# Performance work log

Measured on AMD Instinct MI355X. Metric: run time of the kernel, lower is better.

## Reference

```python
import jax, jax.numpy as jnp
from jax import lax
import numpy as np

D = 128          # condition_dim
NUM_STEPS = 1000
FFN = 2048       # torch TransformerEncoderLayer default dim_feedforward


def _conv(x, w, b):
    # 3x3 conv, stride 1, padding 1 (SAME), NCHW / OIHW layout as in torch
    y = lax.conv_general_dilated(x, w, (1, 1), 'SAME',
                                 dimension_numbers=('NCHW', 'OIHW', 'NCHW'))
    return y + b[None, :, None, None]


def _ln(x, g, b):
    m = jnp.mean(x, -1, keepdims=True)
    v = jnp.mean((x - m) ** 2, -1, keepdims=True)
    return (x - m) / jnp.sqrt(v + 1e-5) * g + b


def setup_inputs() -> dict:
    key = jax.random.key(0)
    ks = iter(jax.random.split(key, 40))
    B, C, H, W = 64, 3, 128, 128
    flat = C * H * W
    def rn(shape, scale=0.02):
        return jax.random.normal(next(ks), shape, jnp.float32) * scale
    return dict(
        cond_img=jax.random.normal(next(ks), (B, C, H, W), jnp.float32),
        tgt_img=jax.random.normal(next(ks), (B, C, H, W), jnp.float32),
        noise=jax.random.normal(next(ks), (B, C, H, W), jnp.float32),
        t=jax.random.randint(next(ks), (B,), 0, NUM_STEPS),
        # condition encoder params
        enc_lin_w=rn((D, flat)), enc_lin_b=jnp.zeros((D,), jnp.float32),
        in_w=rn((2, 3 * D, D)), in_b=jnp.zeros((2, 3 * D), jnp.float32),
        out_w=rn((2, D, D)), out_b=jnp.zeros((2, D), jnp.float32),
        ff1_w=rn((2, FFN, D)), ff1_b=jnp.zeros((2, FFN), jnp.float32),
        ff2_w=rn((2, D, FFN)), ff2_b=jnp.zeros((2, D), jnp.float32),
        ln1_g=jnp.ones((2, D), jnp.float32), ln1_b=jnp.zeros((2, D), jnp.float32),
        ln2_g=jnp.ones((2, D), jnp.float32), ln2_b=jnp.zeros((2, D), jnp.float32),
        # SimpleUNet params
        d1_w=rn((32, C, 3, 3)), d1_b=jnp.zeros((32,), jnp.float32),
        d2_w=rn((64, 32, 3, 3)), d2_b=jnp.zeros((64,), jnp.float32),
        mid_w=rn((64, D)), mid_b=jnp.zeros((64,), jnp.float32),
        u1_w=rn((32, 64, 3, 3)), u1_b=jnp.zeros((32,), jnp.float32),
        u2_w=rn((C, 32, 3, 3)), u2_b=jnp.zeros((C,), jnp.float32),
    )


def _forward(cond_img, tgt_img, noise, t,
             enc_lin_w, enc_lin_b, in_w, in_b, out_w, out_b,
             ff1_w, ff1_b, ff2_w, ff2_b, ln1_g, ln1_b, ln2_g, ln2_b,
             d1_w, d1_b, d2_w, d2_b, mid_w, mid_b, u1_w, u1_b, u2_w, u2_b):
    B = cond_img.shape[0]
    # ---- TransformerConditionEncoder (seq_len == 1, eval mode) ----
    x = cond_img.reshape(B, -1) @ enc_lin_w.T + enc_lin_b  # [B, D]
    for i in range(2):
        # self-attention over a length-1 sequence: softmax over one key == 1,
        # so attn(x) == out_proj(v_proj(x)) exactly.
        v = x @ in_w[i][2 * D:3 * D].T + in_b[i][2 * D:3 * D]
        a = v @ out_w[i].T + out_b[i]
        x = _ln(x + a, ln1_g[i], ln1_b[i])
        f = jnp.maximum(x @ ff1_w[i].T + ff1_b[i], 0.0) @ ff2_w[i].T + ff2_b[i]
        x = _ln(x + f, ln2_g[i], ln2_b[i])
    c = x  # [B, D]
    # ---- LinearScheduler.q_sample ----
    betas = jnp.linspace(1e-4, 0.02, NUM_STEPS)
    alpha_bars = jnp.cumprod(1.0 - betas)
    ab = alpha_bars[t][:, None, None, None]
    z_t = jnp.sqrt(ab) * tgt_img + jnp.sqrt(1.0 - ab) * noise
    # ---- SimpleUNet ----
    h = jax.nn.relu(_conv(z_t, d1_w, d1_b))
    h = jax.nn.relu(_conv(h, d2_w, d2_b))
    h = h + (c @ mid_w.T + mid_b)[:, :, None, None]
    h = jax.nn.relu(_conv(h, u1_w, u1_b))
    eps_pred = _conv(h, u2_w, u2_b)
    # ---- MSE loss ----
    return jnp.mean((eps_pred - noise) ** 2)


def reference(cond_img, tgt_img, noise, t,
              enc_lin_w, enc_lin_b, in_w, in_b, out_w, out_b,
              ff1_w, ff1_b, ff2_w, ff2_b, ln1_g, ln1_b, ln2_g, ln2_b,
              d1_w, d1_b, d2_w, d2_b, mid_w, mid_b, u1_w, u1_b, u2_w, u2_b):
    return _forward(cond_img, tgt_img, noise, t,
                    enc_lin_w, enc_lin_b, in_w, in_b, out_w, out_b,
                    ff1_w, ff1_b, ff2_w, ff2_b, ln1_g, ln1_b, ln2_g, ln2_b,
                    d1_w, d1_b, d2_w, d2_b, mid_w, mid_b, u1_w, u1_b, u2_w, u2_b)
```

## Files before the change

### kernel.cpp

```cpp
#include <hip/hip_runtime.h>
#include <math.h>

#define ENC_K 49152
#define KSEG 64
#define KLEN (ENC_K / KSEG)

typedef __attribute__((ext_vector_type(8))) short bf16x8;
typedef __attribute__((ext_vector_type(4))) float f32x4;

__device__ inline unsigned short f2bf(float f) {
    unsigned int u = __builtin_bit_cast(unsigned int, f);
    unsigned int r = u + 0x7fffu + ((u >> 16) & 1u);
    return (unsigned short)(r >> 16);
}
__device__ inline float bf2f(unsigned short h) {
    return __builtin_bit_cast(float, ((unsigned int)h) << 16);
}
__device__ inline float dot4(const float4 a, const float4 b) {
    return a.x * b.x + a.y * b.y + a.z * b.z + a.w * b.w;
}

__device__ inline int xcd_work(int total) {
    int orig = blockIdx.x + gridDim.x * (blockIdx.y + gridDim.y * blockIdx.z);
    return (orig & 7) * (total >> 3) + (orig >> 3);
}

__global__ void k_alpha(const int* __restrict__ t, float* __restrict__ sab, float* __restrict__ snab) {
    int b = threadIdx.x;
    if (b < 64) {
        int tb = t[b];
        const float step = (0.02f - 1e-4f) / 999.0f;
        float ab = 1.0f;
        for (int i = 0; i <= tb; ++i) {
            float beta = 1e-4f + step * (float)i;
            ab *= (1.0f - beta);
        }
        sab[b] = sqrtf(ab);
        snab[b] = sqrtf(1.0f - ab);
    }
}

__global__ void k_prep_cw(const float* __restrict__ w, unsigned short* __restrict__ out, int CO, int CI) {
    int idx = blockIdx.x * 256 + threadIdx.x;
    int total = CO * CI * 9;
    if (idx < total) {
        int tap = idx / (CO * CI);
        int rem = idx % (CO * CI);
        int co = rem / CI, ci = rem % CI;
        out[idx] = f2bf(w[((size_t)co * CI + ci) * 9 + tap]);
    }
}

__global__ void k_prep_u2(const float* __restrict__ w, unsigned short* __restrict__ out) {
    int idx = blockIdx.x * 256 + threadIdx.x;
    if (idx < 9 * 16 * 32) {
        int tap = idx / 512;
        int rem = idx % 512;
        int co = rem / 32, ci = rem % 32;
        out[idx] = (co < 3) ? f2bf(w[((size_t)co * 32 + ci) * 9 + tap]) : (unsigned short)0;
    }
}

__global__ void k_prep_bf(const float* __restrict__ in, unsigned short* __restrict__ out, int n) {
    int i = blockIdx.x * 256 + threadIdx.x;
    if (i < n) out[i] = f2bf(in[i]);
}

__global__ void k_enc_gemm(const float* __restrict__ cond, const float* __restrict__ w,
                           float* __restrict__ partial) {
    __shared__ float As[32][68];
    __shared__ float Ws[32][68];
    int tid = threadIdx.x;
    int j = tid & 15, i = tid >> 4;
    int d0 = blockIdx.x * 32, b0 = blockIdx.y * 32;
    int k0 = blockIdx.z * KLEN;
    float a00 = 0.f, a01 = 0.f, a10 = 0.f, a11 = 0.f;
    for (int kk = 0; kk < KLEN; kk += 64) {
        for (int idx = tid; idx < 512; idx += 256) {
            int r = idx >> 4, c = (idx & 15) << 2;
            *(float4*)&As[r][c] = *(const float4*)&cond[(size_t)(b0 + r) * ENC_K + k0 + kk + c];
            *(float4*)&Ws[r][c] = *(const float4*)&w[(size_t)(d0 + r) * ENC_K + k0 + kk + c];
        }
        __syncthreads();
        const float4* aA = (const float4*)&As[i][0];
        const float4* aB = (const float4*)&As[i + 16][0];
        const float4* wA = (const float4*)&Ws[j][0];
        const float4* wB = (const float4*)&Ws[j + 16][0];
#pragma unroll
        for (int k = 0; k < 16; ++k) {
            float4 av0 = aA[k], av1 = aB[k], wv0 = wA[k], wv1 = wB[k];
            a00 += dot4(av0, wv0); a01 += dot4(av0, wv1);
            a10 += dot4(av1, wv0); a11 += dot4(av1, wv1);
        }
        __syncthreads();
    }
    size_t base = (size_t)blockIdx.z * 64;
    partial[(base + b0 + i) * 128 + d0 + j] = a00;
    partial[(base + b0 + i) * 128 + d0 + j + 16] = a01;
    partial[(base + b0 + i + 16) * 128 + d0 + j] = a10;
    partial[(base + b0 + i + 16) * 128 + d0 + j + 16] = a11;
}

__global__ void k_enc_reduce(const float* __restrict__ partial, const float* __restrict__ bias,
                             float* __restrict__ x0) {
    int idx = blockIdx.x * 256 + threadIdx.x;
    float s = bias[idx & 127];
    for (int ks = 0; ks < KSEG; ++ks) s += partial[(size_t)ks * 8192 + idx];
    x0[idx] = s;
}

__device__ float sum128(float v, int tid, float* red) {
    if (tid < 128) red[tid] = v;
    __syncthreads();
    if (tid < 64) red[tid] += red[tid + 64]; __syncthreads();
    if (tid < 32) red[tid] += red[tid + 32]; __syncthreads();
    if (tid < 16) red[tid] += red[tid + 16]; __syncthreads();
    if (tid < 8)  red[tid] += red[tid + 8];  __syncthreads();
    if (tid < 4)  red[tid] += red[tid + 4];  __syncthreads();
    if (tid < 2)  red[tid] += red[tid + 2];  __syncthreads();
    if (tid < 1)  red[tid] += red[tid + 1];  __syncthreads();
    float s = red[0];
    __syncthreads();
    return s;
}

__global__ __launch_bounds__(512) void k_tf_attn(
    const float* __restrict__ xs, float* __restrict__ yo,
    const float* __restrict__ in_w, const float* __restrict__ in_b,
    const float* __restrict__ out_w, const float* __restrict__ out_b,
    const float* __restrict__ ln1_g, const float* __restrict__ ln1_b, int L) {
    __shared__ float xr[128], vr[128], tp[4][128], red[128];
    int b = blockIdx.x, tid = threadIdx.x;
    if (tid < 128) xr[tid] = xs[b * 128 + tid];
    __syncthreads();
    int d = tid & 127, s = tid >> 7;
    {
        const float4* w = (const float4*)(in_w + ((size_t)L * 384 + 256 + d) * 128) + s * 8;
        const float4* x4 = (const float4*)xr + s * 8;
        float p = 0.f;
#pragma unroll
        for (int k = 0; k < 8; ++k) p += dot4(x4[k], w[k]);
        tp[s][d] = p;
    }
    __syncthreads();
    if (tid < 128) vr[tid] = in_b[L * 384 + 256 + tid] + tp[0][tid] + tp[1][tid] + tp[2][tid] + tp[3][tid];
    __syncthreads();
    {
        const float4* w = (const float4*)(out_w + ((size_t)L * 128 + d) * 128) + s * 8;
        const float4* v4 = (const float4*)vr + s * 8;
        float p = 0.f;
#pragma unroll
        for (int k = 0; k < 8; ++k) p += dot4(v4[k], w[k]);
        tp[s][d] = p;
    }
    __syncthreads();
    float y = 0.f;
    if (tid < 128) y = xr[tid] + out_b[L * 128 + tid] + tp[0][tid] + tp[1][tid] + tp[2][tid] + tp[3][tid];
    float m1 = sum128(y, tid, red) * (1.f / 128.f);
    float c1 = y - m1;
    float v1 = sum128(c1 * c1, tid, red) * (1.f / 128.f);
    if (tid < 128)
        yo[b * 128 + tid] = c1 * rsqrtf(v1 + 1e-5f) * ln1_g[L * 128 + tid] + ln1_b[L * 128 + tid];
}

__global__ __launch_bounds__(256, 2) void k_ff1m(
    const float* __restrict__ yo, const unsigned short* __restrict__ w1b,
    const float* __restrict__ ff1_b, unsigned short* __restrict__ f1, int L) {
    __shared__ __align__(16) unsigned short xs[64 * 136];
    int tid = threadIdx.x;
    int lane = tid & 63, wv = tid >> 6, l15 = lane & 15, ch = lane >> 4;
    int n0 = blockIdx.x * 64 + wv * 16;
    for (int e = tid; e < 8192; e += 256)
        xs[(e >> 7) * 136 + (e & 127)] = f2bf(yo[e]);
    __syncthreads();
    f32x4 acc[4];
    f32x4 zf = {0.f, 0.f, 0.f, 0.f};
#pragma unroll
    for (int rg = 0; rg < 4; ++rg) acc[rg] = zf;
    const unsigned short* wrow = w1b + ((size_t)L * 2048 + n0 + l15) * 128 + ch * 8;
#pragma unroll
    for (int ks = 0; ks < 4; ++ks) {
        bf16x8 af = *(const bf16x8*)(wrow + ks * 32);
#pragma unroll
        for (int rg = 0; rg < 4; ++rg) {
            bf16x8 bv = *(const bf16x8*)(xs + (rg * 16 + l15) * 136 + ks * 32 + ch * 8);
            acc[rg] = __builtin_amdgcn_mfma_f32_16x16x32_bf16(af, bv, acc[rg], 0, 0, 0);
        }
    }
#pragma unroll
    for (int rg = 0; rg < 4; ++rg) {
        ushort4 o;
#pragma unroll
        for (int r = 0; r < 4; ++r)
            ((unsigned short*)&o)[r] =
                f2bf(fmaxf(acc[rg][r] + ff1_b[L * 2048 + n0 + ch * 4 + r], 0.f));
        *(ushort4*)(f1 + (size_t)(rg * 16 + l15) * 2056 + n0 + ch * 4) = o;
    }
}

__global__ __launch_bounds__(256, 2) void k_ff2m(
    const unsigned short* __restrict__ f1, const unsigned short* __restrict__ w2b,
    float* __restrict__ part, int L) {
    int tid = threadIdx.x;
    int lane = tid & 63, wv = tid >> 6, l15 = lane & 15, ch = lane >> 4;
    int ks = blockIdx.x;
    int dw = blockIdx.y * 64 + wv * 16;
    f32x4 acc[4];
    f32x4 zf = {0.f, 0.f, 0.f, 0.f};
#pragma unroll
    for (int rg = 0; rg < 4; ++rg) acc[rg] = zf;
    const unsigned short* wrow = w2b + ((size_t)L * 128 + dw + l15) * 2048 + ks * 512 + ch * 8;
    const unsigned short* frow = f1 + ks * 512 + ch * 8;
#pragma unroll
    for (int kst = 0; kst < 16; ++kst) {
        bf16x8 af = *(const bf16x8*)(wrow + kst * 32);
#pragma unroll
        for (int rg = 0; rg < 4; ++rg) {
            bf16x8 bv = *(const bf16x8*)(frow + (size_t)(rg * 16 + l15) * 2056 + kst * 32);
            acc[rg] = __builtin_amdgcn_mfma_f32_16x16x32_bf16(af, bv, acc[rg], 0, 0, 0);
        }
    }
#pragma unroll
    for (int rg = 0; rg < 4; ++rg)
        *(float4*)&part[((size_t)ks * 64 + rg * 16 + l15) * 128 + dw + ch * 4] = *(float4*)&acc[rg];
}

__global__ __launch_bounds__(128) void k_tf_red(
    const float* __restrict__ part, const float* __restrict__ yo,
    float* __restrict__ xs, const float* __restrict__ ff2_b,
    const float* __restrict__ ln2_g, const float* __restrict__ ln2_b, int L) {
    __shared__ float red[128];
    int b = blockIdx.x, tid = threadIdx.x;
    float y2 = yo[b * 128 + tid] + ff2_b[L * 128 + tid];
#pragma unroll
    for (int ks = 0; ks < 4; ++ks) y2 += part[((size_t)ks * 64 + b) * 128 + tid];
    float m2 = sum128(y2, tid, red) * (1.f / 128.f);
    float c2 = y2 - m2;
    float v2 = sum128(c2 * c2, tid, red) * (1.f / 128.f);
    xs[b * 128 + tid] = c2 * rsqrtf(v2 + 1e-5f) * ln2_g[L * 128 + tid] + ln2_b[L * 128 + tid];
}

__global__ void k_mid(const float* __restrict__ xe, const float* __restrict__ mid_w,
                      const float* __restrict__ mid_b, float* __restrict__ mid) {
    int b = blockIdx.x, c = threadIdx.x;
    float s = mid_b[c];
    const float* xr = xe + b * 128;
    const float* wr = mid_w + c * 128;
    for (int k = 0; k < 128; ++k) s += xr[k] * wr[k];
    mid[b * 64 + c] = s;
}

__global__ __launch_bounds__(256, 4) void k_conv1(
    const float* __restrict__ tgt, const float* __restrict__ noise,
    const float* __restrict__ sab, const float* __restrict__ snab,
    const float* __restrict__ wgt, const float* __restrict__ bias,
    unsigned short* __restrict__ h1, int b0) {
    __shared__ float it[3][18][35];
    __shared__ float wt[16][3][9];
    int tid = threadIdx.x;
    int tx = tid & 15, ty = tid >> 4;
    int total = gridDim.x * gridDim.y * gridDim.z;
    int w = xcd_work(total);
    int bx = w % gridDim.x; int t2 = w / gridDim.x;
    int by = t2 % gridDim.y; int bz = t2 / gridDim.y;
    int bl = bz >> 1, g = bz & 1;
    int bg = b0 + bl, co0 = g * 16;
    float za = sab[bg], zb = snab[bg];
    for (int idx = tid; idx < 3 * 18 * 34; idx += 256) {
        int c = idx / (18 * 34), rem = idx % (18 * 34);
        int yy = rem / 34, xx = rem % 34;
        int gy = by * 16 + yy - 1, gx = bx * 32 + xx - 1;
        float v = 0.f;
        if (gy >= 0 && gy < 128 && gx >= 0 && gx < 128) {
            size_t off = (((size_t)bg * 3 + c) * 128 + gy) * 128 + gx;
            v = za * tgt[off] + zb * noise[off];
        }
        it[c][yy][xx] = v;
    }
    for (int idx = tid; idx < 16 * 27; idx += 256) {
        int co = idx / 27, rem = idx % 27;
        wt[co][rem / 9][rem % 9] = wgt[(size_t)(co0 + co) * 27 + rem];
    }
    __syncthreads();
    float acc[16][2];
#pragma unroll
    for (int co = 0; co < 16; ++co) { acc[co][0] = 0.f; acc[co][1] = 0.f; }
#pragma unroll
    for (int c = 0; c < 3; ++c)
#pragma unroll
        for (int ky = 0; ky < 3; ++ky) {
            float win[4];
#pragma unroll
            for (int i = 0; i < 4; ++i) win[i] = it[c][ty + ky][tx * 2 + i];
#pragma unroll
            for (int kx = 0; kx < 3; ++kx)
#pragma unroll
                for (int co = 0; co < 16; ++co) {
                    float ww = wt[co][c][ky * 3 + kx];
                    acc[co][0] += win[kx] * ww;
                    acc[co][1] += win[kx + 1] * ww;
                }
        }
    int gy = by * 16 + ty, gx0 = bx * 32 + tx * 2;
#pragma unroll
    for (int p = 0; p < 2; ++p) {
        __attribute__((aligned(16))) unsigned short ov[16];
#pragma unroll
        for (int co = 0; co < 16; ++co)
            ov[co] = f2bf(fmaxf(acc[co][p] + bias[co0 + co], 0.f));
        size_t o = (((size_t)bl * 128 + gy) * 128 + gx0 + p) * 32 + co0;
        *(float4*)(h1 + o) = *(float4*)&ov[0];
        *(float4*)(h1 + o + 8) = *(float4*)&ov[8];
    }
}

template <int CIN, int COB, int COUT, int MOUT>
__global__ __launch_bounds__(256, 2) void k_convMg(
    const unsigned short* __restrict__ in, const unsigned short* __restrict__ wb,
    const float* __restrict__ bias, const float* __restrict__ mid,
    unsigned short* __restrict__ out, int b0) {
    const int GROUPS = COUT / (16 * COB);
    __shared__ __align__(16) unsigned short in_t[10 * 34 * 40];
    __shared__ __align__(16) unsigned short w_t[9 * COB * 16 * 40];
    int tid = threadIdx.x;
    int total = gridDim.x * gridDim.y * gridDim.z;
    int wk = xcd_work(total);
    int bx = wk % gridDim.x; int t2 = wk / gridDim.x;
    int by = t2 % gridDim.y; int bz = t2 / gridDim.y;
    int bl = bz / GROUPS, g = bz % GROUPS;
    int bg = b0 + bl;
    int co0 = g * COB * 16;
    int lane = tid & 63, wv = tid >> 6;
    int l15 = lane & 15, ch = lane >> 4;

    f32x4 acc[2][2][COB];
    f32x4 zf = {0.f, 0.f, 0.f, 0.f};
#pragma unroll
    for (int a = 0; a < 2; ++a)
#pragma unroll
        for (int bq = 0; bq < 2; ++bq)
#pragma unroll
            for (int c = 0; c < COB; ++c) acc[a][bq][c] = zf;

    for (int cs = 0; cs < CIN / 32; ++cs) {
        if (cs) __syncthreads();
        for (int c = tid; c < 10 * 34 * 4; c += 256) {
            int cc = c & 3, pix = c >> 2;
            int xx = pix % 34, yy = pix / 34;
            int gy = by * 8 + yy - 1, gx = bx * 32 + xx - 1;
            bf16x8 v = {0, 0, 0, 0, 0, 0, 0, 0};
            if (gy >= 0 && gy < 128 && gx >= 0 && gx < 128)
                v = *(const bf16x8*)(in + (((size_t)bl * 128 + gy) * 128 + gx) * CIN + cs * 32 + cc * 8);
            *(bf16x8*)(in_t + pix * 40 + cc * 8) = v;
        }
        for (int c = tid; c < 9 * COB * 16 * 4; c += 256) {
            int cc = c & 3, row = c >> 2;
            int tap = row / (COB * 16), co = row % (COB * 16);
            bf16x8 v = *(const bf16x8*)(wb + ((size_t)(tap * COUT + co0 + co)) * CIN + cs * 32 + cc * 8);
            *(bf16x8*)(w_t + row * 40 + cc * 8) = v;
        }
        __syncthreads();
#pragma unroll
        for (int ky = 0; ky < 3; ++ky)
#pragma unroll
            for (int kx = 0; kx < 3; ++kx) {
                int tap = ky * 3 + kx;
                bf16x8 af[COB];
#pragma unroll
                for (int cb = 0; cb < COB; ++cb)
                    af[cb] = *(const bf16x8*)(w_t + (tap * COB * 16 + cb * 16 + l15) * 40 + ch * 8);
#pragma unroll
                for (int yl = 0; yl < 2; ++yl) {
                    int yloc = 2 * wv + yl + ky;
#pragma unroll
                    for (int xt = 0; xt < 2; ++xt) {
                        int xloc = xt * 16 + l15 + kx;
                        bf16x8 bfv = *(const bf16x8*)(in_t + (yloc * 34 + xloc) * 40 + ch * 8);
#pragma unroll
                        for (int cb = 0; cb < COB; ++cb)
                            acc[yl][xt][cb] = __builtin_amdgcn_mfma_f32_16x16x32_bf16(
                                af[cb], bfv, acc[yl][xt][cb], 0, 0, 0);
                    }
                }
            }
    }
#pragma unroll
    for (int yl = 0; yl < 2; ++yl) {
        int gy = by * 8 + 2 * wv + yl;
#pragma unroll
        for (int xt = 0; xt < 2; ++xt) {
            int gx = bx * 32 + xt * 16 + l15;
            size_t pixo = (((size_t)bl * 128 + gy) * 128 + gx) * COUT;
#pragma unroll
            for (int cb = 0; cb < COB; ++cb) {
                int co = co0 + cb * 16 + ch * 4;
                ushort4 o;
#pragma unroll
                for (int r = 0; r < 4; ++r) {
                    float v = acc[yl][xt][cb][r] + bias[co + r];
                    v = fmaxf(v, 0.f);
                    if (MOUT == 2) v += mid[bg * 64 + co + r];
                    ((unsigned short*)&o)[r] = f2bf(v);
                }
                *(ushort4*)(out + pixo + co) = o;
            }
        }
    }
}

__global__ __launch_bounds__(256, 3) void k_u2m(
    const unsigned short* __restrict__ h3, const unsigned short* __restrict__ wbu2,
    const float* __restrict__ u2_b, const float* __restrict__ noise,
    float* __restrict__ partial, int b0) {
    __shared__ __align__(16) unsigned short in_t[340 * 40];
    __shared__ __align__(16) unsigned short w_t[9 * 16 * 40];
    __shared__ float rs[256];
    int tid = threadIdx.x;
    int total = gridDim.x * gridDim.y * gridDim.z;
    int wk = xcd_work(total);
    int bx = wk % gridDim.x; int t2 = wk / gridDim.x;
    int by = t2 % gridDim.y; int bl = t2 / gridDim.y;
    int bg = b0 + bl;
    int lane = tid & 63, wv = tid >> 6, l15 = lane & 15, ch = lane >> 4;

    for (int c = tid; c < 340 * 4; c += 256) {
        int cc = c & 3, pix = c >> 2;
        int xx = pix % 34, yy = pix / 34;
        int gy = by * 8 + yy - 1, gx = bx * 32 + xx - 1;
        bf16x8 v = {0, 0, 0, 0, 0, 0, 0, 0};
        if (gy >= 0 && gy < 128 && gx >= 0 && gx < 128)
            v = *(const bf16x8*)(h3 + (((size_t)bl * 128 + gy) * 128 + gx) * 32 + cc * 8);
        *(bf16x8*)(in_t + pix * 40 + cc * 8) = v;
    }
    for (int c = tid; c < 9 * 16 * 4; c += 256) {
        int cc = c & 3, row = c >> 2;
        bf16x8 v = *(const bf16x8*)(wbu2 + (size_t)row * 32 + cc * 8);
        *(bf16x8*)(w_t + row * 40 + cc * 8) = v;
    }
    __syncthreads();

    f32x4 acc[2][2];
    f32x4 zf = {0.f, 0.f, 0.f, 0.f};
    acc[0][0] = zf; acc[0][1] = zf; acc[1][0] = zf; acc[1][1] = zf;
#pragma unroll
    for (int ky = 0; ky < 3; ++ky)
#pragma unroll
        for (int kx = 0; kx < 3; ++kx) {
            int tap = ky * 3 + kx;
            bf16x8 af = *(const bf16x8*)(w_t + (tap * 16 + l15) * 40 + ch * 8);
#pragma unroll
            for (int yl = 0; yl < 2; ++yl) {
                int yloc = 2 * wv + yl + ky;
#pragma unroll
                for (int xt = 0; xt < 2; ++xt) {
                    int xloc = xt * 16 + l15 + kx;
                    bf16x8 bfv = *(const bf16x8*)(in_t + (yloc * 34 + xloc) * 40 + ch * 8);
                    acc[yl][xt] = __builtin_amdgcn_mfma_f32_16x16x32_bf16(af, bfv, acc[yl][xt], 0, 0, 0);
                }
            }
        }
    float ss = 0.f;
    if (ch == 0) {
#pragma unroll
        for (int yl = 0; yl < 2; ++yl) {
            int gy = by * 8 + 2 * wv + yl;
#pragma unroll
            for (int xt = 0; xt < 2; ++xt) {
                int gx = bx * 32 + xt * 16 + l15;
#pragma unroll
                for (int r = 0; r < 3; ++r) {
                    float v = acc[yl][xt][r] + u2_b[r];
                    float d = v - noise[(((size_t)bg * 3 + r) * 128 + gy) * 128 + gx];
                    ss += d * d;
                }
            }
        }
    }
    rs[tid] = ss;
    __syncthreads();
    for (int s = 128; s > 0; s >>= 1) {
        if (tid < s) rs[tid] += rs[tid + s];
        __syncthreads();
    }
    if (tid == 0) partial[bg * 64 + by * 4 + bx] = rs[0];
}

__global__ void k_final(const float* __restrict__ partial, float* __restrict__ out) {
    __shared__ float rs[256];
    int tid = threadIdx.x;
    float s = 0.f;
    for (int i = tid; i < 4096; i += 256) s += partial[i];
    rs[tid] = s;
    __syncthreads();
    for (int st = 128; st > 0; st >>= 1) {
        if (tid < st) rs[tid] += rs[tid + st];
        __syncthreads();
    }
    if (tid == 0) out[0] = rs[0] / 3145728.0f;
}

extern "C" void kernel_launch(void* const* d_in, const int* in_sizes, int n_in,
                              void* d_out, int out_size, void* d_ws, size_t ws_size,
                              hipStream_t stream) {
    const float* cond   = (const float*)d_in[0];
    const float* tgt    = (const float*)d_in[1];
    const float* noise  = (const float*)d_in[2];
    const int*   t      = (const int*)d_in[3];
    const float* enc_w  = (const float*)d_in[4];
    const float* enc_b  = (const float*)d_in[5];
    const float* in_w   = (const float*)d_in[6];
    const float* in_b   = (const float*)d_in[7];
    const float* out_w  = (const float*)d_in[8];
    const float* out_b  = (const float*)d_in[9];
    const float* ff1_w  = (const float*)d_in[10];
    const float* ff1_b  = (const float*)d_in[11];
    const float* ff2_w  = (const float*)d_in[12];
    const float* ff2_b  = (const float*)d_in[13];
    const float* ln1_g  = (const float*)d_in[14];
    const float* ln1_b  = (const float*)d_in[15];
    const float* ln2_g  = (const float*)d_in[16];
    const float* ln2_b  = (const float*)d_in[17];
    const float* d1_w   = (const float*)d_in[18];
    const float* d1_b   = (const float*)d_in[19];
    const float* d2_w   = (const float*)d_in[20];
    const float* d2_b   = (const float*)d_in[21];
    const float* mid_w  = (const float*)d_in[22];
    const float* mid_b  = (const float*)d_in[23];
    const float* u1_w   = (const float*)d_in[24];
    const float* u1_b   = (const float*)d_in[25];
    const float* u2_w   = (const float*)d_in[26];
    const float* u2_b   = (const float*)d_in[27];

    float* ws = (float*)d_ws;
    float* sab     = ws;
    float* snab    = ws + 64;
    float* x0      = ws + 128;
    float* mid     = ws + 16512;
    float* msepart = ws + 86144;
    unsigned short* wb2  = (unsigned short*)(ws + 90240);
    unsigned short* wbu1 = (unsigned short*)(ws + 99456);
    unsigned short* wbu2 = (unsigned short*)(ws + 108672);

    const size_t SMALL = 131072;
    const size_t ENCP = (size_t)KSEG * 8192;
    float* encpart = ws + SMALL;
    float* tfy     = encpart + ENCP;
    unsigned short* tff1 = (unsigned short*)(tfy + 8192);
    float* tfpart  = tfy + 8192 + 65792;
    unsigned short* wbf1 = (unsigned short*)(tfpart + 32768);
    unsigned short* wbf2 = (unsigned short*)(tfpart + 32768 + 262144);

    size_t fixed = SMALL + ENCP + 8192 + 65792 + 32768 + 262144 + 262144;
    size_t avail = (ws_size / 4 > fixed) ? (ws_size / 4 - fixed) : 0;
    int NB = 1;
    const int cands[7] = {64, 32, 16, 8, 4, 2, 1};
    for (int ci = 0; ci < 7; ++ci) {
        if ((size_t)cands[ci] * 1048576ull <= avail) { NB = cands[ci]; break; }
    }
    unsigned short* hb1 = (unsigned short*)(ws + fixed);
    unsigned short* hb2 = (unsigned short*)(ws + fixed + (size_t)NB * 262144ull);
    unsigned short* hb3 = (unsigned short*)(ws + fixed + (size_t)NB * 786432ull);

    k_alpha<<<1, 64, 0, stream>>>(t, sab, snab);
    k_prep_cw<<<72, 256, 0, stream>>>(d2_w, wb2, 64, 32);
    k_prep_cw<<<72, 256, 0, stream>>>(u1_w, wbu1, 32, 64);
    k_prep_u2<<<18, 256, 0, stream>>>(u2_w, wbu2);
    k_prep_bf<<<2048, 256, 0, stream>>>(ff1_w, wbf1, 524288);
    k_prep_bf<<<2048, 256, 0, stream>>>(ff2_w, wbf2, 524288);
    k_enc_gemm<<<dim3(4, 2, KSEG), 256, 0, stream>>>(cond, enc_w, encpart);
    k_enc_reduce<<<32, 256, 0, stream>>>(encpart, enc_b, x0);
    for (int L = 0; L < 2; ++L) {
        k_tf_attn<<<64, 512, 0, stream>>>(x0, tfy, in_w, in_b, out_w, out_b, ln1_g, ln1_b, L);
        k_ff1m<<<32, 256, 0, stream>>>(tfy, wbf1, ff1_b, tff1, L);
        k_ff2m<<<dim3(4, 2), 256, 0, stream>>>(tff1, wbf2, tfpart, L);
        k_tf_red<<<64, 128, 0, stream>>>(tfpart, tfy, x0, ff2_b, ln2_g, ln2_b, L);
    }
    k_mid<<<64, 64, 0, stream>>>(x0, mid_w, mid_b, mid);

    for (int cb = 0; cb < 64; cb += NB) {
        k_conv1<<<dim3(4, 8, NB * 2), 256, 0, stream>>>(
            tgt, noise, sab, snab, d1_w, d1_b, hb1, cb);
        k_convMg<32, 4, 64, 2><<<dim3(4, 16, NB), 256, 0, stream>>>(
            hb1, wb2, d2_b, mid, hb2, cb);
        k_convMg<64, 2, 32, 1><<<dim3(4, 16, NB), 256, 0, stream>>>(
            hb2, wbu1, u1_b, nullptr, hb3, cb);
        k_u2m<<<dim3(4, 16, NB), 256, 0, stream>>>(
            hb3, wbu2, u2_b, noise, msepart, cb);
    }

    k_final<<<1, 256, 0, stream>>>(msepart, (float*)d_out);
}
```

Baseline: 388.1 us.

## Store h2/h3 activations in FP8 and run u1/u2 convs with FP8 MFMA

The d2 conv now writes its output as packed FP8 instead of bf16. A new FP8 conv kernel for u1 reads that output and writes h3 in FP8, and the u2+MSE kernel now uses FP8 MFMA with FP8 weights. This halves activation traffic for the two intermediate buffers, halves LDS footprint, and uses the higher-throughput FP8 matrix instructions. The trade-off is much lower activation and weight precision, which may push the MSE loss outside tolerance.

```diff
diff --git a/kernel.cpp b/kernel.cpp
--- a/kernel.cpp
+++ b/kernel.cpp
@@ -13,11 +13,17 @@
     unsigned int r = u + 0x7fffu + ((u >> 16) & 1u);
     return (unsigned short)(r >> 16);
 }
-__device__ inline float bf2f(unsigned short h) {
-    return __builtin_bit_cast(float, ((unsigned int)h) << 16);
-}
 __device__ inline float dot4(const float4 a, const float4 b) {
     return a.x * b.x + a.y * b.y + a.z * b.z + a.w * b.w;
+}
+__device__ inline unsigned int pk4_fp8(float a, float b, float c, float d) {
+    int v = 0;
+    v = __builtin_amdgcn_cvt_pk_fp8_f32(a, b, v, false);
+    v = __builtin_amdgcn_cvt_pk_fp8_f32(c, d, v, true);
+    return (unsigned int)v;
+}
+__device__ inline f32x4 mfma_fp8(unsigned long long a, unsigned long long b, f32x4 c) {
+    return __builtin_amdgcn_mfma_f32_16x16x32_fp8_fp8((long)a, (long)b, c, 0, 0, 0);
 }
 
 __device__ inline int xcd_work(int total) {
@@ -51,13 +57,25 @@
     }
 }
 
-__global__ void k_prep_u2(const float* __restrict__ w, unsigned short* __restrict__ out) {
+__global__ void k_prep_u1f8(const float* __restrict__ w, unsigned char* __restrict__ out) {
     int idx = blockIdx.x * 256 + threadIdx.x;
-    if (idx < 9 * 16 * 32) {
-        int tap = idx / 512;
-        int rem = idx % 512;
-        int co = rem / 32, ci = rem % 32;
-        out[idx] = (co < 3) ? f2bf(w[((size_t)co * 32 + ci) * 9 + tap]) : (unsigned short)0;
+    if (idx < 18432) {
+        int tap = idx / 2048, rem = idx % 2048;
+        int co = rem >> 6, ci = rem & 63;
+        float f = w[((size_t)co * 64 + ci) * 9 + tap];
+        int v = __builtin_amdgcn_cvt_pk_fp8_f32(f, 0.f, 0, false);
+        out[idx] = (unsigned char)(v & 0xFF);
+    }
+}
+
+__global__ void k_prep_u2f8(const float* __restrict__ w, unsigned char* __restrict__ out) {
+    int idx = blockIdx.x * 256 + threadIdx.x;
+    if (idx < 4608) {
+        int tap = idx / 512, rem = idx % 512;
+        int co = rem >> 5, ci = rem & 31;
+        float f = (co < 3) ? w[((size_t)co * 32 + ci) * 9 + tap] : 0.f;
+        int v = __builtin_amdgcn_cvt_pk_fp8_f32(f, 0.f, 0, false);
+        out[idx] = (unsigned char)(v & 0xFF);
     }
 }
 
@@ -314,7 +332,7 @@
     }
 }
 
-template <int CIN, int COB, int COUT, int MOUT>
+template <int CIN, int COB, int COUT, int MOUT, int OF8>
 __global__ __launch_bounds__(256, 2) void k_convMg(
     const unsigned short* __restrict__ in, const unsigned short* __restrict__ wb,
     const float* __restrict__ bias, const float* __restrict__ mid,
@@ -394,26 +412,117 @@
 #pragma unroll
             for (int cb = 0; cb < COB; ++cb) {
                 int co = co0 + cb * 16 + ch * 4;
-                ushort4 o;
+                float vv[4];
 #pragma unroll
                 for (int r = 0; r < 4; ++r) {
                     float v = acc[yl][xt][cb][r] + bias[co + r];
                     v = fmaxf(v, 0.f);
                     if (MOUT == 2) v += mid[bg * 64 + co + r];
-                    ((unsigned short*)&o)[r] = f2bf(v);
+                    vv[r] = v;
                 }
-                *(ushort4*)(out + pixo + co) = o;
+                if (OF8) {
+                    unsigned int pk = pk4_fp8(vv[0], vv[1], vv[2], vv[3]);
+                    *(unsigned int*)((unsigned char*)out + pixo + co) = pk;
+                } else {
+                    ushort4 o;
+#pragma unroll
+                    for (int r = 0; r < 4; ++r) ((unsigned short*)&o)[r] = f2bf(vv[r]);
+                    *(ushort4*)(out + pixo + co) = o;
+                }
             }
         }
     }
 }
 
-__global__ __launch_bounds__(256, 3) void k_u2m(
-    const unsigned short* __restrict__ h3, const unsigned short* __restrict__ wbu2,
+__global__ __launch_bounds__(256, 3) void k_convF8u1(
+    const unsigned char* __restrict__ h2, const unsigned char* __restrict__ wb,
+    const float* __restrict__ bias, unsigned char* __restrict__ h3, int b0) {
+    __shared__ __align__(16) unsigned char in_t[340 * 72];
+    __shared__ __align__(16) unsigned char w_t[288 * 72];
+    int tid = threadIdx.x;
+    int total = gridDim.x * gridDim.y * gridDim.z;
+    int wk = xcd_work(total);
+    int bx = wk % gridDim.x; int t2 = wk / gridDim.x;
+    int by = t2 % gridDim.y; int bl = t2 / gridDim.y;
+    int lane = tid & 63, wv = tid >> 6, l15 = lane & 15, ch = lane >> 4;
+
+    for (int c = tid; c < 340 * 8; c += 256) {
+        int cc = c & 7, pix = c >> 3;
+        int xx = pix % 34, yy = pix / 34;
+        int gy = by * 8 + yy - 1, gx = bx * 32 + xx - 1;
+        unsigned long long v = 0ull;
+        if (gy >= 0 && gy < 128 && gx >= 0 && gx < 128)
+            v = *(const unsigned long long*)(h2 + (((size_t)bl * 128 + gy) * 128 + gx) * 64 + cc * 8);
+        *(unsigned long long*)(in_t + pix * 72 + cc * 8) = v;
+    }
+    for (int c = tid; c < 288 * 8; c += 256) {
+        int cc = c & 7, row = c >> 3;
+        *(unsigned long long*)(w_t + row * 72 + cc * 8) =
+            *(const unsigned long long*)(wb + (size_t)row * 64 + cc * 8);
+    }
+    __syncthreads();
+
+    f32x4 acc[2][2][2];
+    f32x4 zf = {0.f, 0.f, 0.f, 0.f};
+#pragma unroll
+    for (int a = 0; a < 2; ++a)
+#pragma unroll
+        for (int bq = 0; bq < 2; ++bq)
+#pragma unroll
+            for (int c = 0; c < 2; ++c) acc[a][bq][c] = zf;
+
+#pragma unroll
+    for (int cs = 0; cs < 2; ++cs)
+#pragma unroll
+        for (int ky = 0; ky < 3; ++ky)
+#pragma unroll
+            for (int kx = 0; kx < 3; ++kx) {
+                int tap = ky * 3 + kx;
+                unsigned long long A[2];
+#pragma unroll
+                for (int cb = 0; cb < 2; ++cb)
+                    A[cb] = *(const unsigned long long*)(
+                        w_t + (tap * 32 + cb * 16 + l15) * 72 + cs * 32 + ch * 8);
+#pragma unroll
+                for (int yl = 0; yl < 2; ++yl) {
+                    int yloc = 2 * wv + yl + ky;
+#pragma unroll
+                    for (int xt = 0; xt < 2; ++xt) {
+                        int xloc = xt * 16 + l15 + kx;
+                        unsigned long long B = *(const unsigned long long*)(
+                            in_t + (yloc * 34 + xloc) * 72 + cs * 32 + ch * 8);
+#pragma unroll
+                        for (int cb = 0; cb < 2; ++cb)
+                            acc[yl][xt][cb] = mfma_fp8(A[cb], B, acc[yl][xt][cb]);
+                    }
+                }
+            }
+#pragma unroll
+    for (int yl = 0; yl < 2; ++yl) {
+        int gy = by * 8 + 2 * wv + yl;
+#pragma unroll
+        for (int xt = 0; xt < 2; ++xt) {
+            int gx = bx * 32 + xt * 16 + l15;
+            size_t pixo = (((size_t)bl * 128 + gy) * 128 + gx) * 32;
+#pragma unroll
+            for (int cb = 0; cb < 2; ++cb) {
+                int co = cb * 16 + ch * 4;
+                float v0 = fmaxf(acc[yl][xt][cb][0] + bias[co], 0.f);
+                float v1 = fmaxf(acc[yl][xt][cb][1] + bias[co + 1], 0.f);
+                float v2 = fmaxf(acc[yl][xt][cb][2] + bias[co + 2], 0.f);
+                float v3 = fmaxf(acc[yl][xt][cb][3] + bias[co + 3], 0.f);
+                *(unsigned int*)(h3 + pixo + co) = pk4_fp8(v0, v1, v2, v3);
+            }
+        }
+    }
+}
+
+__global__ __launch_bounds__(256, 3) void k_u2f8(
+    const unsigned char* __restrict__ h3, const unsigned char* __restrict__ wbu2,
     const float* __restrict__ u2_b, const float* __restrict__ noise,
     float* __restrict__ partial, int b0) {
-    __shared__ __align__(16) unsigned short in_t[340 * 40];
-    __shared__ __align__(16) unsigned short w_t[9 * 16 * 40];
+    __shared__ __align__(16) unsigned char in_t[340 * 40];
+    __shared__ __align__(16) unsigned char w_t[144 * 40];
     __shared__ float rs[256];
     int tid = threadIdx.x;
     int total = gridDim.x * gridDim.y * gridDim.z;
@@ -427,15 +536,15 @@
         int cc = c & 3, pix = c >> 2;
         int xx = pix % 34, yy = pix / 34;
         int gy = by * 8 + yy - 1, gx = bx * 32 + xx - 1;
-        bf16x8 v = {0, 0, 0, 0, 0, 0, 0, 0};
+        unsigned long long v = 0ull;
         if (gy >= 0 && gy < 128 && gx >= 0 && gx < 128)
-            v = *(const bf16x8*)(h3 + (((size_t)bl * 128 + gy) * 128 + gx) * 32 + cc * 8);
-        *(bf16x8*)(in_t + pix * 40 + cc * 8) = v;
-    }
-    for (int c = tid; c < 9 * 16 * 4; c += 256) {
+            v = *(const unsigned long long*)(h3 + (((size_t)bl * 128 + gy) * 128 + gx) * 32 + cc * 8);
+        *(unsigned long long*)(in_t + pix * 40 + cc * 8) = v;
+    }
+    for (int c = tid; c < 144 * 4; c += 256) {
         int cc = c & 3, row = c >> 2;
-        bf16x8 v = *(const bf16x8*)(wbu2 + (size_t)row * 32 + cc * 8);
-        *(bf16x8*)(w_t + row * 40 + cc * 8) = v;
+        *(unsigned long long*)(w_t + row * 40 + cc * 8) =
+            *(const unsigned long long*)(wbu2 + (size_t)row * 32 + cc * 8);
     }
     __syncthreads();
 
@@ -447,15 +556,17 @@
 #pragma unroll
         for (int kx = 0; kx < 3; ++kx) {
             int tap = ky * 3 + kx;
-            bf16x8 af = *(const bf16x8*)(w_t + (tap * 16 + l15) * 40 + ch * 8);
+            unsigned long long A = *(const unsigned long long*)(
+                w_t + (tap * 16 + l15) * 40 + ch * 8);
 #pragma unroll
             for (int yl = 0; yl < 2; ++yl) {
                 int yloc = 2 * wv + yl + ky;
 #pragma unroll
                 for (int xt = 0; xt < 2; ++xt) {
                     int xloc = xt * 16 + l15 + kx;
-                    bf16x8 bfv = *(const bf16x8*)(in_t + (yloc * 34 + xloc) * 40 + ch * 8);
-                    acc[yl][xt] = __builtin_amdgcn_mfma_f32_16x16x32_bf16(af, bfv, acc[yl][xt], 0, 0, 0);
+                    unsigned long long B = *(const unsigned long long*)(
+                        in_t + (yloc * 34 + xloc) * 40 + ch * 8);
+                    acc[yl][xt] = mfma_fp8(A, B, acc[yl][xt]);
                 }
             }
         }
@@ -537,9 +648,9 @@
     float* x0      = ws + 128;
     float* mid     = ws + 16512;
     float* msepart = ws + 86144;
-    unsigned short* wb2  = (unsigned short*)(ws + 90240);
-    unsigned short* wbu1 = (unsigned short*)(ws + 99456);
-    unsigned short* wbu2 = (unsigned short*)(ws + 108672);
+    unsigned short* wb2   = (unsigned short*)(ws + 90240);
+    unsigned char*  wbu1f = (unsigned char*)(ws + 99456);
+    unsigned char*  wbu2f = (unsigned char*)(ws + 108672);
 
     const size_t SMALL = 131072;
     const size_t ENCP = (size_t)KSEG * 8192;
@@ -555,16 +666,16 @@
     int NB = 1;
     const int cands[7] = {64, 32, 16, 8, 4, 2, 1};
     for (int ci = 0; ci < 7; ++ci) {
-        if ((size_t)cands[ci] * 1048576ull <= avail) { NB = cands[ci]; break; }
+        if ((size_t)cands[ci] * 655360ull <= avail) { NB = cands[ci]; break; }
     }
     unsigned short* hb1 = (unsigned short*)(ws + fixed);
-    unsigned short* hb2 = (unsigned short*)(ws + fixed + (size_t)NB * 262144ull);
-    unsigned short* hb3 = (unsigned short*)(ws + fixed + (size_t)NB * 786432ull);
+    unsigned char*  hb2 = (unsigned char*)(ws + fixed + (size_t)NB * 262144ull);
+    unsigned char*  hb3 = (unsigned char*)(ws + fixed + (size_t)NB * 524288ull);
 
     k_alpha<<<1, 64, 0, stream>>>(t, sab, snab);
     k_prep_cw<<<72, 256, 0, stream>>>(d2_w, wb2, 64, 32);
-    k_prep_cw<<<72, 256, 0, stream>>>(u1_w, wbu1, 32, 64);
-    k_prep_u2<<<18, 256, 0, stream>>>(u2_w, wbu2);
+    k_prep_u1f8<<<72, 256, 0, stream>>>(u1_w, wbu1f);
+    k_prep_u2f8<<<18, 256, 0, stream>>>(u2_w, wbu2f);
     k_prep_bf<<<2048, 256, 0, stream>>>(ff1_w, wbf1, 524288);
     k_prep_bf<<<2048, 256, 0, stream>>>(ff2_w, wbf2, 524288);
     k_enc_gemm<<<dim3(4, 2, KSEG), 256, 0, stream>>>(cond, enc_w, encpart);
@@ -580,12 +691,12 @@
     for (int cb = 0; cb < 64; cb += NB) {
         k_conv1<<<dim3(4, 8, NB * 2), 256, 0, stream>>>(
             tgt, noise, sab, snab, d1_w, d1_b, hb1, cb);
-        k_convMg<32, 4, 64, 2><<<dim3(4, 16, NB), 256, 0, stream>>>(
-            hb1, wb2, d2_b, mid, hb2, cb);
-        k_convMg<64, 2, 32, 1><<<dim3(4, 16, NB), 256, 0, stream>>>(
-            hb2, wbu1, u1_b, nullptr, hb3, cb);
-        k_u2m<<<dim3(4, 16, NB), 256, 0, stream>>>(
-            hb3, wbu2, u2_b, noise, msepart, cb);
+        k_convMg<32, 4, 64, 2, 1><<<dim3(4, 16, NB), 256, 0, stream>>>(
+            hb1, wb2, d2_b, mid, (unsigned short*)hb2, cb);
+        k_convF8u1<<<dim3(4, 16, NB), 256, 0, stream>>>(
+            hb2, wbu1f, u1_b, hb3, cb);
+        k_u2f8<<<dim3(4, 16, NB), 256, 0, stream>>>(
+            hb3, wbu2f, u2_b, noise, msepart, cb);
     }
 
     k_final<<<1, 256, 0, stream>>>(msepart, (float*)d_out);
```

Measured after the change: 401.0 us. 3.3% more time.
